# Kernel optimization log

Measured on AMD Instinct MI355X. Metric: run time of the kernel, lower is better.

The kernel has to match this reference:

```python
import jax, jax.numpy as jnp
import numpy as np

N, E = 50000, 800000
IN_F, OUT_F, H = 128, 128, 4
D = OUT_F // H  # head dim
NEG_SLOPE = 0.2
EPS = 1e-12


def setup_inputs() -> dict:
    key = jax.random.key(0)
    ks = jax.random.split(key, 10)
    s = 1.0 / np.sqrt(IN_F)
    return {
        "x": jax.random.normal(ks[0], (N, IN_F), jnp.float32),
        "W_src": jax.random.normal(ks[1], (IN_F, H * D), jnp.float32) * s,
        "b_src": jnp.zeros((H * D,), jnp.float32),
        "W_dst": jax.random.normal(ks[2], (IN_F, H * D), jnp.float32) * s,
        "b_dst": jnp.zeros((H * D,), jnp.float32),
        "attn": jax.random.normal(ks[3], (H, D), jnp.float32) * (1.0 / np.sqrt(D)),
        "out_bias": jnp.zeros((H * D,), jnp.float32),
        "ln_w": jnp.ones((OUT_F,), jnp.float32),
        "ln_b": jnp.zeros((OUT_F,), jnp.float32),
        "src": jax.random.randint(ks[4], (E,), 0, N, jnp.int32),
        "dst": jax.random.randint(ks[5], (E,), 0, N, jnp.int32),
    }


def reference(x, W_src, b_src, W_dst, b_dst, attn, out_bias, ln_w, ln_b, src, dst):
    n = x.shape[0]
    # GATv2Conv (share_weights=False): separate source/dest projections
    fs = (x @ W_src + b_src).reshape(n, H, D)  # [N,H,D]
    fd = (x @ W_dst + b_dst).reshape(n, H, D)
    # per-edge scores: e_ij = attn . leaky_relu(fs[u] + fd[v])
    e = jax.nn.leaky_relu(fs[src] + fd[dst], NEG_SLOPE)  # [E,H,D]
    logits = jnp.einsum("ehd,hd->eh", e, attn)  # [E,H]
    # edge softmax over incoming edges of each dst node
    m = jax.ops.segment_max(logits, dst, num_segments=n)  # [N,H]
    ex = jnp.exp(logits - m[dst])
    denom = jax.ops.segment_sum(ex, dst, num_segments=n)  # [N,H]
    alpha = ex / denom[dst]  # [E,H]
    # aggregate: sum_j alpha_ij * fs[j]
    msg = alpha[:, :, None] * fs[src]  # [E,H,D]
    rst = jax.ops.segment_sum(msg, dst, num_segments=n)  # [N,H,D]
    h = rst.reshape(n, H * D) + out_bias
    # LayerNorm (biased variance, eps inside sqrt)
    u = h.mean(-1, keepdims=True)
    s = jnp.mean((h - u) ** 2, -1, keepdims=True)
    h = (h - u) / jnp.sqrt(s + EPS)
    h = ln_w * h + ln_b
    # activation = elu; dropout p=0 -> identity
    return jax.nn.elu(h)
```

## Files before the change

### kernel.cpp

```cpp
#include <hip/hip_runtime.h>
#include <hip/hip_bf16.h>

constexpr int NF = 128;

using bf16x8 = __attribute__((ext_vector_type(8))) short;
using f32x4v = __attribute__((ext_vector_type(4))) float;

__device__ __forceinline__ unsigned short f2bs(float f) {
    return __builtin_bit_cast(unsigned short, __float2bfloat16(f));
}
__device__ __forceinline__ void unpack8(float4 raw, float* a) {
    unsigned u0 = __float_as_uint(raw.x);
    unsigned u1 = __float_as_uint(raw.y);
    unsigned u2 = __float_as_uint(raw.z);
    unsigned u3 = __float_as_uint(raw.w);
    a[0] = __uint_as_float(u0 << 16);
    a[1] = __uint_as_float(u0 & 0xffff0000u);
    a[2] = __uint_as_float(u1 << 16);
    a[3] = __uint_as_float(u1 & 0xffff0000u);
    a[4] = __uint_as_float(u2 << 16);
    a[5] = __uint_as_float(u2 & 0xffff0000u);
    a[6] = __uint_as_float(u3 << 16);
    a[7] = __uint_as_float(u3 & 0xffff0000u);
}

__global__ void GraphAttnLayer_70196945486348_kernel() {}

__device__ __forceinline__ void gemm_tile(
    const float* __restrict__ x,
    const unsigned short* __restrict__ Wb2,
    const float* __restrict__ bsrc, const float* __restrict__ bdst,
    unsigned short* __restrict__ fs, float* __restrict__ fd,
    int tile, int N)
{
    __shared__ float xs[64][129];
    const int t = threadIdx.x;
    const int lane = t & 63;
    const int wave = t >> 6;
    const int m_base = tile * 64;
    if (m_base >= N) return;
    const int lm = lane & 15;
    const int kq = (lane >> 4) * 8;

    bf16x8 bfrag[4][4];
    float bias[4];
#pragma unroll
    for (int c = 0; c < 4; ++c) {
        int col = wave * 64 + c * 16 + lm;
        bias[c] = (col < 128) ? bsrc[col] : bdst[col - 128];
#pragma unroll
        for (int s = 0; s < 4; ++s)
            bfrag[c][s] = *(const bf16x8*)(Wb2 + ((size_t)((c * 4 + s) * 256 + t)) * 8);
    }

#pragma unroll
    for (int q = 0; q < 8; ++q) {
        int idx = q * 256 + t;
        int row = idx >> 5;
        int c4  = (idx & 31) * 4;
        int grow = m_base + row;
        if (grow >= N) grow = N - 1;
        float4 v = *(const float4*)(x + (size_t)grow * NF + c4);
        xs[row][c4 + 0] = v.x;
        xs[row][c4 + 1] = v.y;
        xs[row][c4 + 2] = v.z;
        xs[row][c4 + 3] = v.w;
    }
    __syncthreads();

    for (int r = 0; r < 4; ++r) {
        int m0 = m_base + r * 16;
        if (m0 >= N) break;
        bf16x8 afrag[4];
#pragma unroll
        for (int s = 0; s < 4; ++s) {
            const float* xp = &xs[r * 16 + lm][s * 32 + kq];
#pragma unroll
            for (int j = 0; j < 8; ++j)
                afrag[s][j] = (short)f2bs(xp[j]);
        }
#pragma unroll
        for (int c = 0; c < 4; ++c) {
            f32x4v acc = {0.f, 0.f, 0.f, 0.f};
#pragma unroll
            for (int s = 0; s < 4; ++s)
                acc = __builtin_amdgcn_mfma_f32_16x16x32_bf16(afrag[s], bfrag[c][s], acc, 0, 0, 0);
            int col = wave * 64 + c * 16 + lm;
            int cc = col & 127;
#pragma unroll
            for (int rr = 0; rr < 4; ++rr) {
                int rowd = m0 + (lane >> 4) * 4 + rr;
                if (rowd < N) {
                    float v = acc[rr] + bias[c];
                    if (col < 128) fs[(size_t)rowd * NF + cc] = f2bs(v);
                    else           fd[(size_t)rowd * NF + cc] = v;
                }
            }
        }
    }
}

__global__ __launch_bounds__(256) void hist_prep_kernel(
    const int* __restrict__ dst,
    int* __restrict__ cntT,
    const float* __restrict__ Wsrc, const float* __restrict__ Wdst,
    unsigned short* __restrict__ Wb2,
    int* __restrict__ state,
    int E, int C, int B, int NSB)
{
    __shared__ int lh[256];
    const int t = threadIdx.x;
    int gi = blockIdx.x * 256 + t;
    if (gi < NSB) state[gi] = 0;
    if (gi < 16 * 256) {
        int j = gi >> 8;
        int tt = gi & 255;
        int wave = tt >> 6;
        int lane = tt & 63;
        int lm = lane & 15;
        int kq = (lane >> 4) * 8;
        int c = j >> 2, s = j & 3;
        int col = wave * 64 + c * 16 + lm;
        int ks = s * 32 + kq;
        bf16x8 frag;
#pragma unroll
        for (int m = 0; m < 8; ++m) {
            float v = (col < 128) ? Wsrc[(ks + m) * NF + col]
                                  : Wdst[(ks + m) * NF + (col - 128)];
            frag[m] = (short)f2bs(v);
        }
        *(bf16x8*)(Wb2 + (size_t)gi * 8) = frag;
    }

    lh[t] = 0;
    __syncthreads();
    int e0 = blockIdx.x * 4096;
    if (e0 + 4096 <= E) {
        const int4* dst4 = (const int4*)(dst + e0);
#pragma unroll
        for (int r = 0; r < 4; ++r) {
            int4 d = dst4[r * 256 + t];
            atomicAdd(&lh[d.x >> 8], 1);
            atomicAdd(&lh[d.y >> 8], 1);
            atomicAdd(&lh[d.z >> 8], 1);
            atomicAdd(&lh[d.w >> 8], 1);
        }
    } else {
#pragma unroll
        for (int j = 0; j < 16; ++j) {
            int e = e0 + j * 256 + t;
            if (e < E) atomicAdd(&lh[dst[e] >> 8], 1);
        }
    }
    __syncthreads();
    if (t < B) cntT[t * C + blockIdx.x] = lh[t];
}

__global__ __launch_bounds__(256) void scan_kernel(
    const int* __restrict__ cntT, int* __restrict__ baseBC,
    int* __restrict__ state, int M)
{
    int b = blockIdx.x, t = threadIdx.x;
    int i = b * 256 + t;
    int v = (i < M) ? cntT[i] : 0;

    __shared__ int arr[256];
    __shared__ int s_bofs;
    arr[t] = v;
    __syncthreads();
    for (int off = 1; off < 256; off <<= 1) {
        int u = (t >= off) ? arr[t - off] : 0;
        __syncthreads();
        arr[t] += u;
        __syncthreads();
    }
    int total = arr[255];

    if (t < 64) {
        if (t == 0) {
            int word = ((b == 0 ? 2 : 1) << 30) | total;
            atomicExch(&state[b], word);
        }
        int bofs = 0;
        if (b > 0) {
            int base = b;
            for (;;) {
                int j = base - 1 - t;
                int sv = 0, f = 1;
                if (j >= 0) {
                    sv = __hip_atomic_load(&state[j], __ATOMIC_RELAXED,
                                           __HIP_MEMORY_SCOPE_AGENT);
                    f = ((unsigned)sv) >> 30;
                }
                unsigned long long notready = __ballot(f == 0);
                if (notready) continue;
                unsigned long long has2 = __ballot(f == 2);
                if (has2) {
                    int k = (int)(__ffsll((unsigned long long)has2) - 1);
                    int val = (t <= k) ? (sv & 0x3FFFFFFF) : 0;
#pragma unroll
                    for (int off = 32; off; off >>= 1) val += __shfl_xor(val, off);
                    bofs += val;
                    break;
                } else {
                    int val = (j >= 0) ? (sv & 0x3FFFFFFF) : 0;
#pragma unroll
                    for (int off = 32; off; off >>= 1) val += __shfl_xor(val, off);
                    bofs += val;
                    base -= 64;
                }
            }
            if (t == 0) atomicExch(&state[b], (2 << 30) | (bofs + total));
        }
        if (t == 0) s_bofs = bofs;
    }
    __syncthreads();
    int excl = arr[t] - v + s_bofs;
    if (i < M) baseBC[i] = excl;
}

__global__ __launch_bounds__(256) void scatter_gemm_kernel(
    const int* __restrict__ dst, const int* __restrict__ src,
    const int* __restrict__ baseBC, unsigned* __restrict__ pairs,
    const float* __restrict__ x, const unsigned short* __restrict__ Wb2,
    const float* __restrict__ bsrc, const float* __restrict__ bdst,
    unsigned short* __restrict__ fs, float* __restrict__ fd,
    int N, int E, int C, int B)
{
    __shared__ int base_lds[256];
    __shared__ int lcnt[256];
    int t = threadIdx.x;
    if (blockIdx.x < (unsigned)C) {
        int chunk = blockIdx.x;
        if (t < B) base_lds[t] = baseBC[t * C + chunk];
        lcnt[t] = 0;
        __syncthreads();
        int e0 = chunk * 4096;
        if (e0 + 4096 <= E) {
            const int4* dst4 = (const int4*)(dst + e0);
            const int4* src4 = (const int4*)(src + e0);
#pragma unroll
            for (int r = 0; r < 4; ++r) {
                int4 d = dst4[r * 256 + t];
                int4 s = src4[r * 256 + t];
                int b0 = d.x >> 8, b1 = d.y >> 8, b2 = d.z >> 8, b3 = d.w >> 8;
                int r0 = atomicAdd(&lcnt[b0], 1);
                int r1 = atomicAdd(&lcnt[b1], 1);
                int r2 = atomicAdd(&lcnt[b2], 1);
                int r3 = atomicAdd(&lcnt[b3], 1);
                pairs[base_lds[b0] + r0] = ((unsigned)(d.x & 255) << 16) | (unsigned)s.x;
                pairs[base_lds[b1] + r1] = ((unsigned)(d.y & 255) << 16) | (unsigned)s.y;
                pairs[base_lds[b2] + r2] = ((unsigned)(d.z & 255) << 16) | (unsigned)s.z;
                pairs[base_lds[b3] + r3] = ((unsigned)(d.w & 255) << 16) | (unsigned)s.w;
            }
        } else {
#pragma unroll
            for (int j = 0; j < 16; ++j) {
                int e = e0 + j * 256 + t;
                if (e < E) {
                    int d = dst[e];
                    int b = d >> 8;
                    int r = atomicAdd(&lcnt[b], 1);
                    pairs[base_lds[b] + r] = ((unsigned)(d & 255) << 16) | (unsigned)src[e];
                }
            }
        }
    } else {
        gemm_tile(x, Wb2, bsrc, bdst, fs, fd, blockIdx.x - C, N);
    }
}

__global__ __launch_bounds__(256) void sort_gemm_kernel(
    const unsigned* __restrict__ pairs, const int* __restrict__ baseBC,
    int* __restrict__ rowptr, unsigned short* __restrict__ src_sorted,
    const float* __restrict__ x, const unsigned short* __restrict__ Wb2,
    const float* __restrict__ bsrc, const float* __restrict__ bdst,
    unsigned short* __restrict__ fs, float* __restrict__ fd,
    int N, int E, int C, int B, int T1)
{
    __shared__ int h[256];
    __shared__ int arr[256];
    __shared__ int cur[256];
    __shared__ unsigned short sorted[16384];
    int t = threadIdx.x;
    if (blockIdx.x < (unsigned)B) {
        int b = blockIdx.x;
        int segbase = baseBC[b * C];
        int end = (b + 1 < B) ? baseBC[(b + 1) * C] : E;
        int count = end - segbase;

        h[t] = 0;
        __syncthreads();
        for (int i = t; i < count; i += 256)
            atomicAdd(&h[pairs[segbase + i] >> 16], 1);
        __syncthreads();
        int v = h[t];
        arr[t] = v;
        __syncthreads();
        for (int off = 1; off < 256; off <<= 1) {
            int u = (t >= off) ? arr[t - off] : 0;
            __syncthreads();
            arr[t] += u;
            __syncthreads();
        }
        int excl = arr[t] - v;
        int node = b * 256 + t;
        if (node <= N) rowptr[node] = segbase + excl;
        cur[t] = excl;
        __syncthreads();
        for (int i = t; i < count; i += 256) {
            unsigned p = pairs[segbase + i];
            int r = atomicAdd(&cur[p >> 16], 1);
            sorted[r] = (unsigned short)(p & 0xFFFF);
        }
        __syncthreads();
        for (int i = t; i < count; i += 256)
            src_sorted[segbase + i] = sorted[i];
    } else {
        gemm_tile(x, Wb2, bsrc, bdst, fs, fd, T1 + (blockIdx.x - B), N);
    }
}

__global__ __launch_bounds__(256) void node_kernel(
    const float4* __restrict__ fsq,
    const int* __restrict__ rowptr, const unsigned short* __restrict__ src_sorted,
    const float4* __restrict__ attn4,
    const float4* __restrict__ obias4,
    const float4* __restrict__ lnw4,
    const float4* __restrict__ lnb4,
    float4* __restrict__ out4, int N)
{
    int lane = threadIdx.x & 63;
    int es = lane >> 4;
    int g  = lane & 15;
    int n = blockIdx.x * 4 + (threadIdx.x >> 6);
    if (n >= N) return;

    float4 fda = out4[(size_t)n * 32 + g * 2];
    float4 fdb = out4[(size_t)n * 32 + g * 2 + 1];
    float4 ava = attn4[g * 2];
    float4 avb = attn4[g * 2 + 1];
    float fd[8] = {fda.x, fda.y, fda.z, fda.w, fdb.x, fdb.y, fdb.z, fdb.w};
    float av[8] = {ava.x, ava.y, ava.z, ava.w, avb.x, avb.y, avb.z, avb.w};

    int beg = rowptr[n], end = rowptr[n + 1];
    float l = 0.f;
    float ac[8] = {0.f, 0.f, 0.f, 0.f, 0.f, 0.f, 0.f, 0.f};

    if (beg < end) {
        int idx = beg + es;
        bool valid = idx < end;
        int s = src_sorted[valid ? idx : (end - 1)];
        float4 raw = fsq[(size_t)s * 16 + g];

        for (int j = beg; j < end; j += 4) {
            int jn = j + 4;
            bool vn = false;
            float4 rawn = raw;
            if (jn < end) {
                int idxn = jn + es;
                vn = idxn < end;
                int sn = src_sorted[vn ? idxn : (end - 1)];
                rawn = fsq[(size_t)sn * 16 + g];
            }

            float a[8];
            unpack8(raw, a);
            float p = 0.f;
#pragma unroll
            for (int d = 0; d < 8; ++d) {
                float t = a[d] + fd[d];
                t = fmaxf(t, 0.2f * t);
                p += av[d] * t;
            }
            p += __shfl_xor(p, 1);
            p += __shfl_xor(p, 2);
            float e = valid ? __expf(p) : 0.f;
            l += e;
#pragma unroll
            for (int d = 0; d < 8; ++d) ac[d] += e * a[d];

            valid = vn;
            raw = rawn;
        }
    }

    l += __shfl_xor(l, 16);
    l += __shfl_xor(l, 32);
#pragma unroll
    for (int d = 0; d < 8; ++d) {
        ac[d] += __shfl_xor(ac[d], 16);
        ac[d] += __shfl_xor(ac[d], 32);
    }

    float rl = (l > 0.f) ? (1.f / l) : 0.f;
    float4 oba = obias4[g * 2];
    float4 obb = obias4[g * 2 + 1];
    float ob[8] = {oba.x, oba.y, oba.z, oba.w, obb.x, obb.y, obb.z, obb.w};
    float h[8];
    float s1 = 0.f, s2 = 0.f;
#pragma unroll
    for (int d = 0; d < 8; ++d) {
        h[d] = ac[d] * rl + ob[d];
        s1 += h[d];
        s2 += h[d] * h[d];
    }
    s1 += __shfl_xor(s1, 1); s2 += __shfl_xor(s2, 1);
    s1 += __shfl_xor(s1, 2); s2 += __shfl_xor(s2, 2);
    s1 += __shfl_xor(s1, 4); s2 += __shfl_xor(s2, 4);
    s1 += __shfl_xor(s1, 8); s2 += __shfl_xor(s2, 8);

    float u = s1 * (1.f / NF);
    float var = s2 * (1.f / NF) - u * u;
    float rstd = rsqrtf(fmaxf(var, 0.f) + 1e-12f);
    float4 gwa = lnw4[g * 2], gwb = lnw4[g * 2 + 1];
    float4 gba = lnb4[g * 2], gbb = lnb4[g * 2 + 1];
    float gw[8] = {gwa.x, gwa.y, gwa.z, gwa.w, gwb.x, gwb.y, gwb.z, gwb.w};
    float gb[8] = {gba.x, gba.y, gba.z, gba.w, gbb.x, gbb.y, gbb.z, gbb.w};
    float z[8];
#pragma unroll
    for (int d = 0; d < 8; ++d) {
        float y = gw[d] * ((h[d] - u) * rstd) + gb[d];
        z[d] = (y > 0.f) ? y : (__expf(y) - 1.f);
    }
    if (es == 0) {
        out4[(size_t)n * 32 + g * 2]     = make_float4(z[0], z[1], z[2], z[3]);
        out4[(size_t)n * 32 + g * 2 + 1] = make_float4(z[4], z[5], z[6], z[7]);
    }
}

extern "C" void kernel_launch(void* const* d_in, const int* in_sizes, int n_in,
                              void* d_out, int out_size, void* d_ws, size_t ws_size,
                              hipStream_t stream)
{
    const float* x    = (const float*)d_in[0];
    const float* Wsrc = (const float*)d_in[1];
    const float* bsrc = (const float*)d_in[2];
    const float* Wdst = (const float*)d_in[3];
    const float* bdst = (const float*)d_in[4];
    const float4* attn4 = (const float4*)d_in[5];
    const float4* obias4= (const float4*)d_in[6];
    const float4* lnw4  = (const float4*)d_in[7];
    const float4* lnb4  = (const float4*)d_in[8];
    const int* src = (const int*)d_in[9];
    const int* dst = (const int*)d_in[10];
    int N = in_sizes[0] / NF;
    int E = in_sizes[9];

    int C = (E + 4095) / 4096;
    int B = (N + 255) / 256;
    int M = B * C;
    int NSB = (M + 255) / 256;
    int T = (N + 63) / 64;
    int T1 = (T * 5) / 8;
    int T2 = T - T1;

    int* cntT = (int*)d_ws;
    int* baseBC = cntT + M;
    int* state = baseBC + M;
    int* rowptr = state + 256;
    unsigned* pairs = (unsigned*)(rowptr + (N + 1));
    unsigned short* srcs = (unsigned short*)(pairs + E);
    unsigned short* Wb2 = srcs + ((E + 1) & ~1);
    unsigned short* fs = Wb2 + 16 * 256 * 8;

    hist_prep_kernel<<<C, 256, 0, stream>>>(dst, cntT, Wsrc, Wdst, Wb2,
                                            state, E, C, B, NSB);
    scan_kernel<<<NSB, 256, 0, stream>>>(cntT, baseBC, state, M);
    scatter_gemm_kernel<<<C + T1, 256, 0, stream>>>(
        dst, src, baseBC, pairs, x, Wb2, bsrc, bdst, fs, (float*)d_out,
        N, E, C, B);
    sort_gemm_kernel<<<B + T2, 256, 0, stream>>>(
        pairs, baseBC, rowptr, srcs, x, Wb2, bsrc, bdst, fs, (float*)d_out,
        N, E, C, B, T1);
    node_kernel<<<(N + 3) / 4, 256, 0, stream>>>(
        (const float4*)fs, rowptr, srcs, attn4, obias4, lnw4, lnb4,
        (float4*)d_out, N);
}
```

Before: 177.5 us.

## Replace decoupled-lookback multi-block scan with single-block scan; unroll sort loops

Replaces the multi-block decoupled-lookback prefix scan, which needed a state array cleared in the histogram kernel and spin-waiting across blocks, with a single 1024-thread block where each thread serially scans a contiguous slice. This removes inter-block polling and the state buffer, at the cost of running the scan on one CU with serial per-thread loops over strided global reads (M = 196*196, about 38K entries, roughly 38 per thread). It also unrolls the histogram and counting-sort loops in the sort kernel by four so several pair loads are in flight before the LDS atomics.

```diff
diff --git a/kernel.cpp b/kernel.cpp
--- a/kernel.cpp
+++ b/kernel.cpp
@@ -105,13 +105,11 @@
     int* __restrict__ cntT,
     const float* __restrict__ Wsrc, const float* __restrict__ Wdst,
     unsigned short* __restrict__ Wb2,
-    int* __restrict__ state,
-    int E, int C, int B, int NSB)
+    int E, int C, int B)
 {
     __shared__ int lh[256];
     const int t = threadIdx.x;
     int gi = blockIdx.x * 256 + t;
-    if (gi < NSB) state[gi] = 0;
     if (gi < 16 * 256) {
         int j = gi >> 8;
         int tt = gi & 255;
@@ -156,67 +154,31 @@
     if (t < B) cntT[t * C + blockIdx.x] = lh[t];
 }
 
-__global__ __launch_bounds__(256) void scan_kernel(
-    const int* __restrict__ cntT, int* __restrict__ baseBC,
-    int* __restrict__ state, int M)
-{
-    int b = blockIdx.x, t = threadIdx.x;
-    int i = b * 256 + t;
-    int v = (i < M) ? cntT[i] : 0;
-
-    __shared__ int arr[256];
-    __shared__ int s_bofs;
-    arr[t] = v;
+__global__ __launch_bounds__(1024) void scan_kernel(
+    const int* __restrict__ cntT, int* __restrict__ baseBC, int M)
+{
+    __shared__ int ws[1024];
+    int t = threadIdx.x;
+    int per = (M + 1023) / 1024;
+    int beg = t * per;
+    int end = beg + per; if (end > M) end = M;
+
+    int sum = 0;
+    for (int i = beg; i < end; ++i) sum += cntT[i];
+    ws[t] = sum;
     __syncthreads();
-    for (int off = 1; off < 256; off <<= 1) {
-        int u = (t >= off) ? arr[t - off] : 0;
-        __syncthreads();
-        arr[t] += u;
-        __syncthreads();
-    }
-    int total = arr[255];
-
-    if (t < 64) {
-        if (t == 0) {
-            int word = ((b == 0 ? 2 : 1) << 30) | total;
-            atomicExch(&state[b], word);
-        }
-        int bofs = 0;
-        if (b > 0) {
-            int base = b;
-            for (;;) {
-                int j = base - 1 - t;
-                int sv = 0, f = 1;
-                if (j >= 0) {
-                    sv = __hip_atomic_load(&state[j], __ATOMIC_RELAXED,
-                                           __HIP_MEMORY_SCOPE_AGENT);
-                    f = ((unsigned)sv) >> 30;
-                }
-                unsigned long long notready = __ballot(f == 0);
-                if (notready) continue;
-                unsigned long long has2 = __ballot(f == 2);
-                if (has2) {
-                    int k = (int)(__ffsll((unsigned long long)has2) - 1);
-                    int val = (t <= k) ? (sv & 0x3FFFFFFF) : 0;
-#pragma unroll
-                    for (int off = 32; off; off >>= 1) val += __shfl_xor(val, off);
-                    bofs += val;
-                    break;
-                } else {
-                    int val = (j >= 0) ? (sv & 0x3FFFFFFF) : 0;
-#pragma unroll
-                    for (int off = 32; off; off >>= 1) val += __shfl_xor(val, off);
-                    bofs += val;
-                    base -= 64;
-                }
-            }
-            if (t == 0) atomicExch(&state[b], (2 << 30) | (bofs + total));
-        }
-        if (t == 0) s_bofs = bofs;
-    }
-    __syncthreads();
-    int excl = arr[t] - v + s_bofs;
-    if (i < M) baseBC[i] = excl;
+    for (int off = 1; off < 1024; off <<= 1) {
+        int u = (t >= off) ? ws[t - off] : 0;
+        __syncthreads();
+        ws[t] += u;
+        __syncthreads();
+    }
+    int run = ws[t] - sum;
+    for (int i = beg; i < end; ++i) {
+        int v = cntT[i];
+        baseBC[i] = run;
+        run += v;
+    }
 }
 
 __global__ __launch_bounds__(256) void scatter_gemm_kernel(
@@ -291,8 +253,21 @@
 
         h[t] = 0;
         __syncthreads();
-        for (int i = t; i < count; i += 256)
-            atomicAdd(&h[pairs[segbase + i] >> 16], 1);
+        {
+            int i = t;
+            for (; i + 768 < count; i += 1024) {
+                unsigned p0 = pairs[segbase + i];
+                unsigned p1 = pairs[segbase + i + 256];
+                unsigned p2 = pairs[segbase + i + 512];
+                unsigned p3 = pairs[segbase + i + 768];
+                atomicAdd(&h[p0 >> 16], 1);
+                atomicAdd(&h[p1 >> 16], 1);
+                atomicAdd(&h[p2 >> 16], 1);
+                atomicAdd(&h[p3 >> 16], 1);
+            }
+            for (; i < count; i += 256)
+                atomicAdd(&h[pairs[segbase + i] >> 16], 1);
+        }
         __syncthreads();
         int v = h[t];
         arr[t] = v;
@@ -308,10 +283,27 @@
         if (node <= N) rowptr[node] = segbase + excl;
         cur[t] = excl;
         __syncthreads();
-        for (int i = t; i < count; i += 256) {
-            unsigned p = pairs[segbase + i];
-            int r = atomicAdd(&cur[p >> 16], 1);
-            sorted[r] = (unsigned short)(p & 0xFFFF);
+        {
+            int i = t;
+            for (; i + 768 < count; i += 1024) {
+                unsigned p0 = pairs[segbase + i];
+                unsigned p1 = pairs[segbase + i + 256];
+                unsigned p2 = pairs[segbase + i + 512];
+                unsigned p3 = pairs[segbase + i + 768];
+                int r0 = atomicAdd(&cur[p0 >> 16], 1);
+                int r1 = atomicAdd(&cur[p1 >> 16], 1);
+                int r2 = atomicAdd(&cur[p2 >> 16], 1);
+                int r3 = atomicAdd(&cur[p3 >> 16], 1);
+                sorted[r0] = (unsigned short)(p0 & 0xFFFF);
+                sorted[r1] = (unsigned short)(p1 & 0xFFFF);
+                sorted[r2] = (unsigned short)(p2 & 0xFFFF);
+                sorted[r3] = (unsigned short)(p3 & 0xFFFF);
+            }
+            for (; i < count; i += 256) {
+                unsigned p = pairs[segbase + i];
+                int r = atomicAdd(&cur[p >> 16], 1);
+                sorted[r] = (unsigned short)(p & 0xFFFF);
+            }
         }
         __syncthreads();
         for (int i = t; i < count; i += 256)
@@ -450,23 +442,21 @@
     int C = (E + 4095) / 4096;
     int B = (N + 255) / 256;
     int M = B * C;
-    int NSB = (M + 255) / 256;
     int T = (N + 63) / 64;
     int T1 = (T * 5) / 8;
     int T2 = T - T1;
 
     int* cntT = (int*)d_ws;
     int* baseBC = cntT + M;
-    int* state = baseBC + M;
-    int* rowptr = state + 256;
+    int* rowptr = baseBC + M;
     unsigned* pairs = (unsigned*)(rowptr + (N + 1));
     unsigned short* srcs = (unsigned short*)(pairs + E);
     unsigned short* Wb2 = srcs + ((E + 1) & ~1);
     unsigned short* fs = Wb2 + 16 * 256 * 8;
 
     hist_prep_kernel<<<C, 256, 0, stream>>>(dst, cntT, Wsrc, Wdst, Wb2,
-                                            state, E, C, B, NSB);
-    scan_kernel<<<NSB, 256, 0, stream>>>(cntT, baseBC, state, M);
+                                            E, C, B);
+    scan_kernel<<<1, 1024, 0, stream>>>(cntT, baseBC, M);
     scatter_gemm_kernel<<<C + T1, 256, 0, stream>>>(
         dst, src, baseBC, pairs, x, Wb2, bsrc, bdst, fs, (float*)d_out,
         N, E, C, B);
```

After: 224.9 us. +26.7%, slower.
